# Kernel optimization log

Hardware: AMD Instinct MI355X
Metric: run time of the kernel (lower is better)

Reference implementation:

```python
import jax, jax.numpy as jnp
import numpy as np

B, N, D_PTS, D_MODEL, K = 2, 8192, 3, 128, 16


def _gather(points, idx):
    # points: (B, N, C), idx: (B, M, K) -> (B, M, K, C)
    return jax.vmap(lambda p, i: p[i])(points, idx)


def setup_inputs() -> dict:
    key = jax.random.key(0)
    ks = jax.random.split(key, 20)

    def w(k, shape, fan_in):
        bound = 1.0 / np.sqrt(fan_in)
        return jax.random.uniform(k, shape, jnp.float32, -bound, bound)

    return {
        "xyz": jax.random.normal(ks[0], (B, D_PTS, N), jnp.float32),
        "features": jax.random.normal(ks[1], (B, D_PTS, N), jnp.float32),
        "fc1_w": w(ks[2], (D_MODEL, D_PTS), D_PTS),
        "fc1_b": w(ks[3], (D_MODEL,), D_PTS),
        "fc2_w": w(ks[4], (D_PTS, D_MODEL), D_MODEL),
        "fc2_b": w(ks[5], (D_PTS,), D_MODEL),
        "d1_w": w(ks[6], (D_MODEL, 3), 3),
        "d1_b": w(ks[7], (D_MODEL,), 3),
        "d2_w": w(ks[8], (D_MODEL, D_MODEL), D_MODEL),
        "d2_b": w(ks[9], (D_MODEL,), D_MODEL),
        "g1_w": w(ks[10], (D_MODEL, D_MODEL), D_MODEL),
        "g1_b": w(ks[11], (D_MODEL,), D_MODEL),
        "g2_w": w(ks[12], (D_MODEL, D_MODEL), D_MODEL),
        "g2_b": w(ks[13], (D_MODEL,), D_MODEL),
        "wq_w": w(ks[14], (D_MODEL, D_MODEL), D_MODEL),
        "wk_w": w(ks[15], (D_MODEL, D_MODEL), D_MODEL),
        "wv_w": w(ks[16], (D_MODEL, D_MODEL), D_MODEL),
    }


def reference(xyz, features, fc1_w, fc1_b, fc2_w, fc2_b,
              d1_w, d1_b, d2_w, d2_b, g1_w, g1_b, g2_w, g2_b,
              wq_w, wk_w, wv_w):
    xyz_p = jnp.swapaxes(xyz, 1, 2)        # (B, N, 3)
    feat = jnp.swapaxes(features, 1, 2)    # (B, N, d_points)

    # square_distance(xyz, xyz): ||a||^2 + ||b||^2 - 2 a.b
    sq = jnp.sum(xyz_p * xyz_p, axis=-1)   # (B, N)
    dists = sq[:, :, None] + sq[:, None, :] - 2.0 * jnp.einsum('bnc,bmc->bnm', xyz_p, xyz_p)
    _, knn_idx = jax.lax.top_k(-dists, K)  # (B, N, K) indices of k smallest dists

    knn_xyz = _gather(xyz_p, knn_idx)      # (B, N, K, 3)
    pre = feat

    x = feat @ fc1_w.T + fc1_b             # (B, N, d_model)
    q = x @ wq_w.T                         # (B, N, d_model)
    kg = _gather(x @ wk_w.T, knn_idx)      # (B, N, K, d_model)
    vg = _gather(x @ wv_w.T, knn_idx)      # (B, N, K, d_model)

    rel = xyz_p[:, :, None] - knn_xyz      # (B, N, K, 3)
    pos = jax.nn.relu(rel @ d1_w.T + d1_b) @ d2_w.T + d2_b          # fc_delta

    h = q[:, :, None] - kg + pos
    attn = jax.nn.relu(h @ g1_w.T + g1_b) @ g2_w.T + g2_b           # fc_gamma
    attn = jax.nn.softmax(attn / np.sqrt(D_MODEL), axis=-2)         # softmax over K

    res = jnp.einsum('bmnf,bmnf->bmf', attn, vg + pos)              # (B, N, d_model)
    res = res @ fc2_w.T + fc2_b + pre                               # (B, N, d_points)
    return jnp.swapaxes(res, 1, 2)                                  # (B, d_points, N)
```

## Files before the change

kernel.cpp:

```cpp
#include <hip/hip_runtime.h>
#include <cfloat>

#define NPTS 8192

typedef __attribute__((ext_vector_type(8))) short short8;
typedef __attribute__((ext_vector_type(4))) short short4v;
typedef __attribute__((ext_vector_type(4))) float f32x4;

__device__ inline unsigned short f2bf(float f) {
    unsigned u = __builtin_bit_cast(unsigned, f);
    u += 0x7fffu + ((u >> 16) & 1u);
    return (unsigned short)(u >> 16);
}
__device__ inline float bf2f(unsigned short h) {
    unsigned u = ((unsigned)h) << 16;
    return __builtin_bit_cast(float, u);
}

__global__ void prep_kernel(const float* __restrict__ d2_w,
                            const float* __restrict__ g1_w,
                            const float* __restrict__ g2_w,
                            unsigned short* __restrict__ wd2,
                            unsigned short* __restrict__ wg1,
                            unsigned short* __restrict__ wg2,
                            const float* __restrict__ xyz,
                            float4* __restrict__ candp,
                            const float* __restrict__ wq_w,
                            const float* __restrict__ wk_w,
                            const float* __restrict__ wv_w,
                            float* __restrict__ wqT,
                            float* __restrict__ wkT,
                            float* __restrict__ wvT)
{
    int i = blockIdx.x * 256 + threadIdx.x;
    if (i < 49152) {
        int sel = i >> 14, off = i & 16383;
        const float* s = (sel == 0) ? d2_w : (sel == 1) ? g1_w : g2_w;
        unsigned short* d = (sel == 0) ? wd2 : (sel == 1) ? wg1 : wg2;
        d[off] = f2bf(s[off]);
    } else if (i < 65536) {
        int j = i - 49152;
        int b = j >> 13, n = j & 8191;
        const float* xg = xyz + (long)b * 3 * NPTS;
        float x = xg[n], y = xg[NPTS + n], z = xg[2*NPTS + n];
        float4 c; c.x = x; c.y = y; c.z = z;
        c.w = fmaf(x, x, fmaf(y, y, z * z));
        candp[j] = c;
    } else if (i < 114688) {
        int idx = i - 65536;
        int sel = idx >> 14, off = idx & 16383;
        int k = off >> 7, c = off & 127;
        const float* s = (sel == 0) ? wq_w : (sel == 1) ? wk_w : wv_w;
        float* d = (sel == 0) ? wqT : (sel == 1) ? wkT : wvT;
        d[off] = s[c * 128 + k];
    }
}

__global__ __launch_bounds__(128, 2)
void proj_kernel(const float* __restrict__ feat,
                 const float* __restrict__ fc1_w, const float* __restrict__ fc1_b,
                 const float* __restrict__ wqT, const float* __restrict__ wkT,
                 const float* __restrict__ wvT,
                 unsigned short* __restrict__ qb, unsigned short* __restrict__ kbuf,
                 unsigned short* __restrict__ vbuf)
{
    __shared__ float fl[8][3];
    __shared__ float xl[8][128];
    const int c = threadIdx.x;
    const long base = (long)blockIdx.x * 8;

    if (c < 24) {
        int p = c / 3, d = c % 3;
        long pt = base + p;
        int b = (int)(pt >> 13), n = (int)(pt & 8191);
        fl[p][d] = feat[((long)b * 3 + d) * NPTS + n];
    }
    __syncthreads();

    float w0 = fc1_w[c*3+0], w1 = fc1_w[c*3+1], w2 = fc1_w[c*3+2], b0 = fc1_b[c];
    #pragma unroll
    for (int p = 0; p < 8; ++p)
        xl[p][c] = fmaf(w0, fl[p][0], fmaf(w1, fl[p][1], fmaf(w2, fl[p][2], b0)));
    __syncthreads();

    float aq[8], ak[8], av[8];
    #pragma unroll
    for (int p = 0; p < 8; ++p) { aq[p] = 0.f; ak[p] = 0.f; av[p] = 0.f; }

    for (int i4 = 0; i4 < 32; ++i4) {
        const int k0 = i4 * 4;
        float qa = wqT[(k0+0)*128 + c], qbw = wqT[(k0+1)*128 + c];
        float qc2 = wqT[(k0+2)*128 + c], qd = wqT[(k0+3)*128 + c];
        float ka = wkT[(k0+0)*128 + c], kbw = wkT[(k0+1)*128 + c];
        float kc2 = wkT[(k0+2)*128 + c], kd = wkT[(k0+3)*128 + c];
        float va = wvT[(k0+0)*128 + c], vbw = wvT[(k0+1)*128 + c];
        float vc2 = wvT[(k0+2)*128 + c], vd = wvT[(k0+3)*128 + c];
        #pragma unroll
        for (int p = 0; p < 8; ++p) {
            float4 x = *(const float4*)&xl[p][k0];
            aq[p] = fmaf(qa,x.x, fmaf(qbw,x.y, fmaf(qc2,x.z, fmaf(qd,x.w, aq[p]))));
            ak[p] = fmaf(ka,x.x, fmaf(kbw,x.y, fmaf(kc2,x.z, fmaf(kd,x.w, ak[p]))));
            av[p] = fmaf(va,x.x, fmaf(vbw,x.y, fmaf(vc2,x.z, fmaf(vd,x.w, av[p]))));
        }
    }
    const int perm = (c & 15) * 8 + (c >> 4);
    #pragma unroll
    for (int p = 0; p < 8; ++p) {
        long pt = base + p;
        qb[pt*128 + perm]   = f2bf(aq[p]);
        kbuf[pt*128 + perm] = f2bf(ak[p]);
        vbuf[pt*128 + perm] = f2bf(av[p]);
    }
}

#define KNB 120
#define KBBASE 952
#define KCAP 64

__global__ __launch_bounds__(512, 6)
void knn_part_kernel(const float4* __restrict__ cand,
                     float* __restrict__ part_d, int* __restrict__ part_i)
{
    __shared__ unsigned hist[KNB * 64];
    __shared__ float2   surv[64 * 65];
    __shared__ unsigned scnt[64];
    __shared__ int      bthr[64];

    const int t  = threadIdx.x;
    const int ql = t & 63, wv = t >> 6;
    const int wv_u = __builtin_amdgcn_readfirstlane(wv);
    const int qsg = blockIdx.x >> 1;
    const int ck  = blockIdx.x & 1;
    const int b_u = qsg >> 7;
    const int q   = qsg * 64 + ql;
    const int n   = q & 8191;

    const float4* cp = cand + (b_u << 13) + ck * 4096 + wv_u * 512;
    const int ibase = ck * 4096 + wv_u * 512;
    float4 qc = cand[(b_u << 13) + n];
    const float qx2 = -2.f * qc.x, qy2 = -2.f * qc.y, qz2 = -2.f * qc.z;
    const float qw = qc.w;

    for (int i = t; i < KNB * 64; i += 512) hist[i] = 0u;
    if (t < 64) scnt[t] = 0u;
    __syncthreads();

    auto dtil = [&](float4 c) {
        return fmaf(qx2, c.x, fmaf(qy2, c.y, fmaf(qz2, c.z, c.w + qw)));
    };
    auto binOf = [&](float d) {
        float dc = fmaxf(d, 1e-30f);
        int b = (int)(__builtin_bit_cast(unsigned, dc) >> 20) - KBBASE;
        return b < 0 ? 0 : (b > (KNB - 1) ? (KNB - 1) : b);
    };

    {
        unsigned* hq = hist + ql;
        float4 A[8], Bv[8];
        #pragma unroll
        for (int u = 0; u < 8; ++u) A[u] = cp[u];
        for (int m = 0; m < 512; m += 16) {
            #pragma unroll
            for (int u = 0; u < 8; ++u) Bv[u] = cp[m + 8 + u];
            #pragma unroll
            for (int u = 0; u < 8; ++u) {
                int bb = binOf(dtil(A[u]));
                atomicAdd(hq + bb * 64, 1u);
            }
            if (m + 16 < 512) {
                #pragma unroll
                for (int u = 0; u < 8; ++u) A[u] = cp[m + 16 + u];
            }
            #pragma unroll
            for (int u = 0; u < 8; ++u) {
                int bb = binOf(dtil(Bv[u]));
                atomicAdd(hq + bb * 64, 1u);
            }
        }
    }
    __syncthreads();

    if (t < 64) {
        int cum = 0, bs = 0;
        #pragma unroll 8
        for (int b = 0; b < KNB; ++b) {
            cum += (int)hist[b * 64 + t];
            bs += (cum < 16) ? 1 : 0;
        }
        bthr[t] = (bs >= KNB - 1) ? 0x7FFFFFFF : ((bs + KBBASE + 1) << 20);
    }
    __syncthreads();

    {
        const int mythr = bthr[ql];
        float4 A[8], Bv[8];
        #pragma unroll
        for (int u = 0; u < 8; ++u) A[u] = cp[u];
        for (int m = 0; m < 512; m += 16) {
            #pragma unroll
            for (int u = 0; u < 8; ++u) Bv[u] = cp[m + 8 + u];
            #pragma unroll
            for (int u = 0; u < 8; ++u) {
                float d = dtil(A[u]);
                if (__builtin_bit_cast(int, d) < mythr) {
                    unsigned s = atomicAdd(&scnt[ql], 1u);
                    if (s < (unsigned)KCAP) {
                        float2 e; e.x = d;
                        e.y = __builtin_bit_cast(float, ibase + m + u);
                        surv[ql * 65 + s] = e;
                    }
                }
            }
            if (m + 16 < 512) {
                #pragma unroll
                for (int u = 0; u < 8; ++u) A[u] = cp[m + 16 + u];
            }
            #pragma unroll
            for (int u = 0; u < 8; ++u) {
                float d = dtil(Bv[u]);
                if (__builtin_bit_cast(int, d) < mythr) {
                    unsigned s = atomicAdd(&scnt[ql], 1u);
                    if (s < (unsigned)KCAP) {
                        float2 e; e.x = d;
                        e.y = __builtin_bit_cast(float, ibase + m + 8 + u);
                        surv[ql * 65 + s] = e;
                    }
                }
            }
        }
    }
    __syncthreads();

    {
        const int q2 = t >> 3;
        const int s0 = t & 7;
        const unsigned cnt = min(scnt[q2], (unsigned)KCAP);
        const float2* sp = surv + q2 * 65;
        const long pb = ((long)(qsg * 64 + q2)) * 32 + ck * 16;
        for (unsigned s = s0; s < cnt; s += 8) {
            float2 e = sp[s];
            float d = e.x;
            int idx = __builtin_bit_cast(int, e.y);
            int rank = 0;
            #pragma unroll 8
            for (unsigned j = 0; j < cnt; ++j) {
                float2 f = sp[j];
                float dj = f.x;
                int ij = __builtin_bit_cast(int, f.y);
                rank += ((dj < d) || (dj == d && ij < idx)) ? 1 : 0;
            }
            if (rank < 16) {
                part_d[pb + rank] = d;
                part_i[pb + rank] = idx;
            }
        }
    }
}

__global__ __launch_bounds__(256, 4)
void knn_merge_kernel(const float* __restrict__ part_d,
                      const int* __restrict__ part_i, int* __restrict__ knn)
{
    __shared__ float sd[8][33];
    __shared__ int   si[8][33];
    const int t = threadIdx.x;
    const int qq = t >> 5, e = t & 31;
    const long q = (long)blockIdx.x * 8 + qq;
    float d = part_d[q * 32 + e];
    int idx = part_i[q * 32 + e];
    sd[qq][e] = d; si[qq][e] = idx;
    __syncthreads();
    int rank = 0;
    #pragma unroll
    for (int j = 0; j < 32; ++j) {
        float dj = sd[qq][j];
        rank += ((dj < d) || (dj == d && si[qq][j] < idx)) ? 1 : 0;
    }
    if (rank < 16) knn[q * 16 + rank] = idx;
}

__device__ inline int hswz(int r, int c) {
    return r * 128 + (c ^ ((r & 7) << 4));
}

__global__ __launch_bounds__(64, 2)
void attn_kernel(const float* __restrict__ xyz, const float* __restrict__ feat,
                 const float* __restrict__ d1_w, const float* __restrict__ d1_b,
                 const float* __restrict__ d2_b, const float* __restrict__ g1_b,
                 const float* __restrict__ g2_b,
                 const float* __restrict__ fc2_w, const float* __restrict__ fc2_b,
                 const unsigned short* __restrict__ qb,
                 const unsigned short* __restrict__ kb,
                 const unsigned short* __restrict__ vb,
                 const unsigned short* __restrict__ wd2,
                 const unsigned short* __restrict__ wg1,
                 const unsigned short* __restrict__ wg2,
                 const int* __restrict__ knn, float* __restrict__ out)
{
    __shared__ unsigned short hbuf[32 * 128];

    const int lane = threadIdx.x;
    const int quad = lane >> 4, l15 = lane & 15;
    const long pbase = (long)blockIdx.x * 2;
    const int b = (int)(pbase >> 13);
    const long bofs = (long)b * NPTS;

    int m = 0; float rx = 0.f, ry = 0.f, rz = 0.f;
    if (lane < 32) {
        m = knn[(pbase + (lane >> 4)) * 16 + (lane & 15)];
        int nn = (int)((pbase + (lane >> 4)) & 8191);
        const float* xg = xyz + (long)b * 3 * NPTS;
        rx = xg[nn]        - xg[m];
        ry = xg[NPTS+nn]   - xg[NPTS+m];
        rz = xg[2*NPTS+nn] - xg[2*NPTS+m];
    }

    int koff[8];
    #pragma unroll
    for (int mt = 0; mt < 2; ++mt)
        #pragma unroll
        for (int r = 0; r < 4; ++r) {
            int idxm = __shfl(m, mt*16 + quad*4 + r);
            koff[mt*4 + r] = (int)(bofs + idxm) * 128 + l15*8;
        }

    short8 qvv[2], kgv[2][4], vgv[2][4];
    #pragma unroll
    for (int mt = 0; mt < 2; ++mt) {
        qvv[mt] = *(const short8*)(qb + (size_t)(pbase + mt) * 128 + l15*8);
        #pragma unroll
        for (int r = 0; r < 4; ++r)
            kgv[mt][r] = *(const short8*)(kb + koff[mt*4 + r]);
    }

    {
        float w0[8], w1[8], w2[8], bb[8];
        #pragma unroll
        for (int k = 0; k < 8; ++k) {
            int c = l15*8 + k;
            w0[k] = d1_w[c*3]; w1[k] = d1_w[c*3+1]; w2[k] = d1_w[c*3+2];
            bb[k] = d1_b[c];
        }
        #pragma unroll
        for (int i = 0; i < 8; ++i) {
            int row = quad + 4*i;
            float sx = __shfl(rx, row), sy = __shfl(ry, row), sz = __shfl(rz, row);
            short8 hv;
            #pragma unroll
            for (int k = 0; k < 8; ++k) {
                float v = fmaf(w0[k], sx, fmaf(w1[k], sy, fmaf(w2[k], sz, bb[k])));
                hv[k] = (short)f2bf(fmaxf(v, 0.f));
            }
            *(short8*)&hbuf[hswz(row, l15*8)] = hv;
        }
    }

    short8 A[2][4];
    f32x4 acc[2];

    auto loadA = [&]() {
        #pragma unroll
        for (int mt = 0; mt < 2; ++mt)
            #pragma unroll
            for (int kk = 0; kk < 4; ++kk)
                A[mt][kk] = *(const short8*)&hbuf[hswz(mt*16 + l15, kk*32 + quad*8)];
    };

    unsigned posp[2][8][2];

    loadA();
    #pragma unroll
    for (int n0 = 0; n0 < 8; ++n0) {
        const unsigned short* wp = wd2 + (n0*16 + l15) * 128 + quad*8;
        short8 B0 = *(const short8*)(wp);
        short8 B1 = *(const short8*)(wp + 32);
        short8 B2 = *(const short8*)(wp + 64);
        short8 B3 = *(const short8*)(wp + 96);
        acc[0] = (f32x4){0.f,0.f,0.f,0.f};
        acc[1] = (f32x4){0.f,0.f,0.f,0.f};
        __builtin_amdgcn_s_setprio(1);
        #pragma unroll
        for (int mt = 0; mt < 2; ++mt) {
            acc[mt] = __builtin_amdgcn_mfma_f32_16x16x32_bf16(A[mt][0], B0, acc[mt], 0, 0, 0);
            acc[mt] = __builtin_amdgcn_mfma_f32_16x16x32_bf16(A[mt][1], B1, acc[mt], 0, 0, 0);
            acc[mt] = __builtin_amdgcn_mfma_f32_16x16x32_bf16(A[mt][2], B2, acc[mt], 0, 0, 0);
            acc[mt] = __builtin_amdgcn_mfma_f32_16x16x32_bf16(A[mt][3], B3, acc[mt], 0, 0, 0);
        }
        __builtin_amdgcn_s_setprio(0);
        int c = n0*16 + l15;
        float bb = d2_b[c];
        #pragma unroll
        for (int mt = 0; mt < 2; ++mt) {
            float qv = bf2f((unsigned short)qvv[mt][n0]);
            float p0 = acc[mt][0] + bb, p1 = acc[mt][1] + bb;
            float p2 = acc[mt][2] + bb, p3 = acc[mt][3] + bb;
            posp[mt][n0][0] = (unsigned)f2bf(p0) | ((unsigned)f2bf(p1) << 16);
            posp[mt][n0][1] = (unsigned)f2bf(p2) | ((unsigned)f2bf(p3) << 16);
            int rb = mt*16 + quad*4;
            hbuf[hswz(rb+0, c)] = f2bf(qv - bf2f((unsigned short)kgv[mt][0][n0]) + p0);
            hbuf[hswz(rb+1, c)] = f2bf(qv - bf2f((unsigned short)kgv[mt][1][n0]) + p1);
            hbuf[hswz(rb+2, c)] = f2bf(qv - bf2f((unsigned short)kgv[mt][2][n0]) + p2);
            hbuf[hswz(rb+3, c)] = f2bf(qv - bf2f((unsigned short)kgv[mt][3][n0]) + p3);
        }
    }

    loadA();
    #pragma unroll
    for (int n0 = 0; n0 < 8; ++n0) {
        const unsigned short* wp = wg1 + (n0*16 + l15) * 128 + quad*8;
        short8 B0 = *(const short8*)(wp);
        short8 B1 = *(const short8*)(wp + 32);
        short8 B2 = *(const short8*)(wp + 64);
        short8 B3 = *(const short8*)(wp + 96);
        acc[0] = (f32x4){0.f,0.f,0.f,0.f};
        acc[1] = (f32x4){0.f,0.f,0.f,0.f};
        __builtin_amdgcn_s_setprio(1);
        #pragma unroll
        for (int mt = 0; mt < 2; ++mt) {
            acc[mt] = __builtin_amdgcn_mfma_f32_16x16x32_bf16(A[mt][0], B0, acc[mt], 0, 0, 0);
            acc[mt] = __builtin_amdgcn_mfma_f32_16x16x32_bf16(A[mt][1], B1, acc[mt], 0, 0, 0);
            acc[mt] = __builtin_amdgcn_mfma_f32_16x16x32_bf16(A[mt][2], B2, acc[mt], 0, 0, 0);
            acc[mt] = __builtin_amdgcn_mfma_f32_16x16x32_bf16(A[mt][3], B3, acc[mt], 0, 0, 0);
        }
        __builtin_amdgcn_s_setprio(0);
        int c = n0*16 + l15;
        float bb = g1_b[c];
        #pragma unroll
        for (int mt = 0; mt < 2; ++mt) {
            int rb = mt*16 + quad*4;
            #pragma unroll
            for (int r = 0; r < 4; ++r)
                hbuf[hswz(rb+r, c)] = f2bf(fmaxf(acc[mt][r] + bb, 0.f));
        }
    }

    #pragma unroll
    for (int mt = 0; mt < 2; ++mt)
        #pragma unroll
        for (int r = 0; r < 4; ++r)
            vgv[mt][r] = *(const short8*)(vb + koff[mt*4 + r]);

    loadA();
    const float sc = 0.08838834764831845f;
    float pr[2][3];
    #pragma unroll
    for (int mt = 0; mt < 2; ++mt) { pr[mt][0] = 0.f; pr[mt][1] = 0.f; pr[mt][2] = 0.f; }
    #pragma unroll
    for (int n0 = 0; n0 < 8; ++n0) {
        const unsigned short* wp = wg2 + (n0*16 + l15) * 128 + quad*8;
        short8 B0 = *(const short8*)(wp);
        short8 B1 = *(const short8*)(wp + 32);
        short8 B2 = *(const short8*)(wp + 64);
        short8 B3 = *(const short8*)(wp + 96);
        acc[0] = (f32x4){0.f,0.f,0.f,0.f};
        acc[1] = (f32x4){0.f,0.f,0.f,0.f};
        __builtin_amdgcn_s_setprio(1);
        #pragma unroll
        for (int mt = 0; mt < 2; ++mt) {
            acc[mt] = __builtin_amdgcn_mfma_f32_16x16x32_bf16(A[mt][0], B0, acc[mt], 0, 0, 0);
            acc[mt] = __builtin_amdgcn_mfma_f32_16x16x32_bf16(A[mt][1], B1, acc[mt], 0, 0, 0);
            acc[mt] = __builtin_amdgcn_mfma_f32_16x16x32_bf16(A[mt][2], B2, acc[mt], 0, 0, 0);
            acc[mt] = __builtin_amdgcn_mfma_f32_16x16x32_bf16(A[mt][3], B3, acc[mt], 0, 0, 0);
        }
        __builtin_amdgcn_s_setprio(0);
        int c = n0*16 + l15;
        float bb = g2_b[c];
        float f0 = fc2_w[c];
        float f1 = fc2_w[128 + c];
        float f2 = fc2_w[256 + c];
        #pragma unroll
        for (int mt = 0; mt < 2; ++mt) {
            float e0 = (acc[mt][0] + bb) * sc;
            float e1 = (acc[mt][1] + bb) * sc;
            float e2 = (acc[mt][2] + bb) * sc;
            float e3 = (acc[mt][3] + bb) * sc;
            float mx = fmaxf(fmaxf(e0, e1), fmaxf(e2, e3));
            mx = fmaxf(mx, __shfl_xor(mx, 16));
            mx = fmaxf(mx, __shfl_xor(mx, 32));
            e0 = __expf(e0 - mx); e1 = __expf(e1 - mx);
            e2 = __expf(e2 - mx); e3 = __expf(e3 - mx);
            float ssum = e0 + e1 + e2 + e3;
            ssum += __shfl_xor(ssum, 16);
            ssum += __shfl_xor(ssum, 32);
            float p0 = bf2f((unsigned short)(posp[mt][n0][0] & 0xffff));
            float p1 = bf2f((unsigned short)(posp[mt][n0][0] >> 16));
            float p2 = bf2f((unsigned short)(posp[mt][n0][1] & 0xffff));
            float p3 = bf2f((unsigned short)(posp[mt][n0][1] >> 16));
            float p = e0 * (bf2f((unsigned short)vgv[mt][0][n0]) + p0)
                    + e1 * (bf2f((unsigned short)vgv[mt][1][n0]) + p1)
                    + e2 * (bf2f((unsigned short)vgv[mt][2][n0]) + p2)
                    + e3 * (bf2f((unsigned short)vgv[mt][3][n0]) + p3);
            p += __shfl_xor(p, 16);
            p += __shfl_xor(p, 32);
            float rres = p / ssum;
            pr[mt][0] = fmaf(f0, rres, pr[mt][0]);
            pr[mt][1] = fmaf(f1, rres, pr[mt][1]);
            pr[mt][2] = fmaf(f2, rres, pr[mt][2]);
        }
    }

    #pragma unroll
    for (int mt = 0; mt < 2; ++mt) {
        float pr0 = pr[mt][0], pr1 = pr[mt][1], pr2 = pr[mt][2];
        #pragma unroll
        for (int s2 = 1; s2 <= 8; s2 <<= 1) {
            pr0 += __shfl_xor(pr0, s2);
            pr1 += __shfl_xor(pr1, s2);
            pr2 += __shfl_xor(pr2, s2);
        }
        int nn = (int)((pbase + mt) & 8191);
        if (lane < 3) {
            float pv = (lane == 0) ? pr0 : (lane == 1) ? pr1 : pr2;
            long o = ((long)b*3 + lane) * NPTS + nn;
            out[o] = pv + fc2_b[lane] + feat[o];
        }
    }
}

extern "C" void kernel_launch(void* const* d_in, const int* in_sizes, int n_in,
                              void* d_out, int out_size, void* d_ws, size_t ws_size,
                              hipStream_t stream)
{
    const float* xyz   = (const float*)d_in[0];
    const float* feat  = (const float*)d_in[1];
    const float* fc1_w = (const float*)d_in[2];
    const float* fc1_b = (const float*)d_in[3];
    const float* fc2_w = (const float*)d_in[4];
    const float* fc2_b = (const float*)d_in[5];
    const float* d1_w  = (const float*)d_in[6];
    const float* d1_b  = (const float*)d_in[7];
    const float* d2_w  = (const float*)d_in[8];
    const float* d2_b  = (const float*)d_in[9];
    const float* g1_w  = (const float*)d_in[10];
    const float* g1_b  = (const float*)d_in[11];
    const float* g2_w  = (const float*)d_in[12];
    const float* g2_b  = (const float*)d_in[13];
    const float* wq_w  = (const float*)d_in[14];
    const float* wk_w  = (const float*)d_in[15];
    const float* wv_w  = (const float*)d_in[16];
    float* out = (float*)d_out;

    unsigned short* qb  = (unsigned short*)d_ws;
    unsigned short* kb  = qb + (size_t)16384*128;
    unsigned short* vb  = kb + (size_t)16384*128;
    unsigned short* wd2 = vb + (size_t)16384*128;
    unsigned short* wg1 = wd2 + 16384;
    unsigned short* wg2 = wg1 + 16384;
    int*   knn_ws = (int*)(wg2 + 16384);
    float4* cand  = (float4*)(knn_ws + (size_t)16384*16);
    float* part_d = (float*)(cand + 16384);
    int*   part_i = (int*)(part_d + (size_t)16384*64);
    float* wqT    = part_d + (size_t)16384*32;
    float* wkT    = wqT + 16384;
    float* wvT    = wkT + 16384;

    hipLaunchKernelGGL(prep_kernel, dim3(448), dim3(256), 0, stream,
                       d2_w, g1_w, g2_w, wd2, wg1, wg2, xyz, cand,
                       wq_w, wk_w, wv_w, wqT, wkT, wvT);
    hipLaunchKernelGGL(knn_part_kernel, dim3(512), dim3(512), 0, stream,
                       cand, part_d, part_i);
    hipLaunchKernelGGL(knn_merge_kernel, dim3(2048), dim3(256), 0, stream,
                       part_d, part_i, knn_ws);
    hipLaunchKernelGGL(proj_kernel, dim3(2048), dim3(128), 0, stream,
                       feat, fc1_w, fc1_b, wqT, wkT, wvT, qb, kb, vb);
    hipLaunchKernelGGL(attn_kernel, dim3(8192), dim3(64), 0, stream,
                       xyz, feat, d1_w, d1_b, d2_b, g1_b, g2_b, fc2_w, fc2_b,
                       qb, kb, vb, wd2, wg1, wg2, knn_ws, out);
}
```

Measured before the change: 313.6 us.

## Merge kNN partial search and QKV projection into one heterogeneous launch

Fuses the kNN partial kernel and the QKV projection kernel into a single launch. The first 512 blocks do kNN and the remaining 512 blocks do the projection, with 4 groups of 8 points per block and shared memory unioned between the two roles. The aim is to run the independent projection work alongside kNN and drop one launch. In exchange, launch bounds drop from 6 to 2 blocks per CU for the kNN part, which may reduce its occupancy, and the projection blocks now carry the larger shared-memory footprint.

New measurement: 296.6 us. 5.4% less time.

```diff
diff --git a/kernel.cpp b/kernel.cpp
--- a/kernel.cpp
+++ b/kernel.cpp
@@ -56,203 +56,222 @@
     }
 }
 
-__global__ __launch_bounds__(128, 2)
-void proj_kernel(const float* __restrict__ feat,
-                 const float* __restrict__ fc1_w, const float* __restrict__ fc1_b,
-                 const float* __restrict__ wqT, const float* __restrict__ wkT,
-                 const float* __restrict__ wvT,
-                 unsigned short* __restrict__ qb, unsigned short* __restrict__ kbuf,
-                 unsigned short* __restrict__ vbuf)
-{
-    __shared__ float fl[8][3];
-    __shared__ float xl[8][128];
-    const int c = threadIdx.x;
-    const long base = (long)blockIdx.x * 8;
-
-    if (c < 24) {
-        int p = c / 3, d = c % 3;
-        long pt = base + p;
-        int b = (int)(pt >> 13), n = (int)(pt & 8191);
-        fl[p][d] = feat[((long)b * 3 + d) * NPTS + n];
-    }
-    __syncthreads();
-
-    float w0 = fc1_w[c*3+0], w1 = fc1_w[c*3+1], w2 = fc1_w[c*3+2], b0 = fc1_b[c];
-    #pragma unroll
-    for (int p = 0; p < 8; ++p)
-        xl[p][c] = fmaf(w0, fl[p][0], fmaf(w1, fl[p][1], fmaf(w2, fl[p][2], b0)));
-    __syncthreads();
-
-    float aq[8], ak[8], av[8];
-    #pragma unroll
-    for (int p = 0; p < 8; ++p) { aq[p] = 0.f; ak[p] = 0.f; av[p] = 0.f; }
-
-    for (int i4 = 0; i4 < 32; ++i4) {
-        const int k0 = i4 * 4;
-        float qa = wqT[(k0+0)*128 + c], qbw = wqT[(k0+1)*128 + c];
-        float qc2 = wqT[(k0+2)*128 + c], qd = wqT[(k0+3)*128 + c];
-        float ka = wkT[(k0+0)*128 + c], kbw = wkT[(k0+1)*128 + c];
-        float kc2 = wkT[(k0+2)*128 + c], kd = wkT[(k0+3)*128 + c];
-        float va = wvT[(k0+0)*128 + c], vbw = wvT[(k0+1)*128 + c];
-        float vc2 = wvT[(k0+2)*128 + c], vd = wvT[(k0+3)*128 + c];
-        #pragma unroll
-        for (int p = 0; p < 8; ++p) {
-            float4 x = *(const float4*)&xl[p][k0];
-            aq[p] = fmaf(qa,x.x, fmaf(qbw,x.y, fmaf(qc2,x.z, fmaf(qd,x.w, aq[p]))));
-            ak[p] = fmaf(ka,x.x, fmaf(kbw,x.y, fmaf(kc2,x.z, fmaf(kd,x.w, ak[p]))));
-            av[p] = fmaf(va,x.x, fmaf(vbw,x.y, fmaf(vc2,x.z, fmaf(vd,x.w, av[p]))));
-        }
-    }
-    const int perm = (c & 15) * 8 + (c >> 4);
-    #pragma unroll
-    for (int p = 0; p < 8; ++p) {
-        long pt = base + p;
-        qb[pt*128 + perm]   = f2bf(aq[p]);
-        kbuf[pt*128 + perm] = f2bf(ak[p]);
-        vbuf[pt*128 + perm] = f2bf(av[p]);
-    }
-}
-
 #define KNB 120
 #define KBBASE 952
 #define KCAP 64
 
-__global__ __launch_bounds__(512, 6)
-void knn_part_kernel(const float4* __restrict__ cand,
-                     float* __restrict__ part_d, int* __restrict__ part_i)
+__global__ __launch_bounds__(512, 2)
+void knn_proj_kernel(const float4* __restrict__ cand,
+                     float* __restrict__ part_d, int* __restrict__ part_i,
+                     const float* __restrict__ feat,
+                     const float* __restrict__ fc1_w, const float* __restrict__ fc1_b,
+                     const float* __restrict__ wqT, const float* __restrict__ wkT,
+                     const float* __restrict__ wvT,
+                     unsigned short* __restrict__ qb,
+                     unsigned short* __restrict__ kbuf,
+                     unsigned short* __restrict__ vbuf)
 {
-    __shared__ unsigned hist[KNB * 64];
-    __shared__ float2   surv[64 * 65];
-    __shared__ unsigned scnt[64];
-    __shared__ int      bthr[64];
-
-    const int t  = threadIdx.x;
-    const int ql = t & 63, wv = t >> 6;
-    const int wv_u = __builtin_amdgcn_readfirstlane(wv);
-    const int qsg = blockIdx.x >> 1;
-    const int ck  = blockIdx.x & 1;
-    const int b_u = qsg >> 7;
-    const int q   = qsg * 64 + ql;
-    const int n   = q & 8191;
-
-    const float4* cp = cand + (b_u << 13) + ck * 4096 + wv_u * 512;
-    const int ibase = ck * 4096 + wv_u * 512;
-    float4 qc = cand[(b_u << 13) + n];
-    const float qx2 = -2.f * qc.x, qy2 = -2.f * qc.y, qz2 = -2.f * qc.z;
-    const float qw = qc.w;
-
-    for (int i = t; i < KNB * 64; i += 512) hist[i] = 0u;
-    if (t < 64) scnt[t] = 0u;
-    __syncthreads();
-
-    auto dtil = [&](float4 c) {
-        return fmaf(qx2, c.x, fmaf(qy2, c.y, fmaf(qz2, c.z, c.w + qw)));
-    };
-    auto binOf = [&](float d) {
-        float dc = fmaxf(d, 1e-30f);
-        int b = (int)(__builtin_bit_cast(unsigned, dc) >> 20) - KBBASE;
-        return b < 0 ? 0 : (b > (KNB - 1) ? (KNB - 1) : b);
-    };
-
-    {
-        unsigned* hq = hist + ql;
-        float4 A[8], Bv[8];
-        #pragma unroll
-        for (int u = 0; u < 8; ++u) A[u] = cp[u];
-        for (int m = 0; m < 512; m += 16) {
+    __shared__ union {
+        struct {
+            unsigned hist[KNB * 64];
+            float2   surv[64 * 65];
+            unsigned scnt[64];
+            int      bthr[64];
+        } k;
+        struct {
+            float fl[32][3];
+            float xl[32][128];
+        } p;
+    } sm;
+
+    const int t = threadIdx.x;
+
+    if (blockIdx.x < 512) {
+        unsigned* hist = sm.k.hist;
+        float2*   surv = sm.k.surv;
+        unsigned* scnt = sm.k.scnt;
+        int*      bthr = sm.k.bthr;
+
+        const int ql = t & 63, wv = t >> 6;
+        const int wv_u = __builtin_amdgcn_readfirstlane(wv);
+        const int qsg = blockIdx.x >> 1;
+        const int ck  = blockIdx.x & 1;
+        const int b_u = qsg >> 7;
+        const int q   = qsg * 64 + ql;
+        const int n   = q & 8191;
+
+        const float4* cp = cand + (b_u << 13) + ck * 4096 + wv_u * 512;
+        const int ibase = ck * 4096 + wv_u * 512;
+        float4 qc = cand[(b_u << 13) + n];
+        const float qx2 = -2.f * qc.x, qy2 = -2.f * qc.y, qz2 = -2.f * qc.z;
+        const float qw = qc.w;
+
+        for (int i = t; i < KNB * 64; i += 512) hist[i] = 0u;
+        if (t < 64) scnt[t] = 0u;
+        __syncthreads();
+
+        auto dtil = [&](float4 c) {
+            return fmaf(qx2, c.x, fmaf(qy2, c.y, fmaf(qz2, c.z, c.w + qw)));
+        };
+        auto binOf = [&](float d) {
+            float dc = fmaxf(d, 1e-30f);
+            int b = (int)(__builtin_bit_cast(unsigned, dc) >> 20) - KBBASE;
+            return b < 0 ? 0 : (b > (KNB - 1) ? (KNB - 1) : b);
+        };
+
+        {
+            unsigned* hq = hist + ql;
+            float4 A[8], Bv[8];
             #pragma unroll
-            for (int u = 0; u < 8; ++u) Bv[u] = cp[m + 8 + u];
+            for (int u = 0; u < 8; ++u) A[u] = cp[u];
+            for (int m = 0; m < 512; m += 16) {
+                #pragma unroll
+                for (int u = 0; u < 8; ++u) Bv[u] = cp[m + 8 + u];
+                #pragma unroll
+                for (int u = 0; u < 8; ++u) {
+                    int bb = binOf(dtil(A[u]));
+                    atomicAdd(hq + bb * 64, 1u);
+                }
+                if (m + 16 < 512) {
+                    #pragma unroll
+                    for (int u = 0; u < 8; ++u) A[u] = cp[m + 16 + u];
+                }
+                #pragma unroll
+                for (int u = 0; u < 8; ++u) {
+                    int bb = binOf(dtil(Bv[u]));
+                    atomicAdd(hq + bb * 64, 1u);
+                }
+            }
+        }
+        __syncthreads();
+
+        if (t < 64) {
+            int cum = 0, bs = 0;
+            #pragma unroll 8
+            for (int b = 0; b < KNB; ++b) {
+                cum += (int)hist[b * 64 + t];
+                bs += (cum < 16) ? 1 : 0;
+            }
+            bthr[t] = (bs >= KNB - 1) ? 0x7FFFFFFF : ((bs + KBBASE + 1) << 20);
+        }
+        __syncthreads();
+
+        {
+            const int mythr = bthr[ql];
+            float4 A[8], Bv[8];
             #pragma unroll
-            for (int u = 0; u < 8; ++u) {
-                int bb = binOf(dtil(A[u]));
-                atomicAdd(hq + bb * 64, 1u);
+            for (int u = 0; u < 8; ++u) A[u] = cp[u];
+            for (int m = 0; m < 512; m += 16) {
+                #pragma unroll
+                for (int u = 0; u < 8; ++u) Bv[u] = cp[m + 8 + u];
+                #pragma unroll
+                for (int u = 0; u < 8; ++u) {
+                    float d = dtil(A[u]);
+                    if (__builtin_bit_cast(int, d) < mythr) {
+                        unsigned s = atomicAdd(&scnt[ql], 1u);
+                        if (s < (unsigned)KCAP) {
+                            float2 e; e.x = d;
+                            e.y = __builtin_bit_cast(float, ibase + m + u);
+                            surv[ql * 65 + s] = e;
+                        }
+                    }
+                }
+                if (m + 16 < 512) {
+                    #pragma unroll
+                    for (int u = 0; u < 8; ++u) A[u] = cp[m + 16 + u];
+                }
+                #pragma unroll
+                for (int u = 0; u < 8; ++u) {
+                    float d = dtil(Bv[u]);
+                    if (__builtin_bit_cast(int, d) < mythr) {
+                        unsigned s = atomicAdd(&scnt[ql], 1u);
+                        if (s < (unsigned)KCAP) {
+                            float2 e; e.x = d;
+                            e.y = __builtin_bit_cast(float, ibase + m + 8 + u);
+                            surv[ql * 65 + s] = e;
+                        }
+                    }
+                }
             }
-            if (m + 16 < 512) {
-                #pragma unroll
-                for (int u = 0; u < 8; ++u) A[u] = cp[m + 16 + u];
+        }
+        __syncthreads();
+
+        {
+            const int q2 = t >> 3;
+            const int s0 = t & 7;
+            const unsigned cnt = min(scnt[q2], (unsigned)KCAP);
+            const float2* sp = surv + q2 * 65;
+            const long pb = ((long)(qsg * 64 + q2)) * 32 + ck * 16;
+            for (unsigned s = s0; s < cnt; s += 8) {
+                float2 e = sp[s];
+                float d = e.x;
+                int idx = __builtin_bit_cast(int, e.y);
+                int rank = 0;
+                #pragma unroll 8
+                for (unsigned j = 0; j < cnt; ++j) {
+                    float2 f = sp[j];
+                    float dj = f.x;
+                    int ij = __builtin_bit_cast(int, f.y);
+                    rank += ((dj < d) || (dj == d && ij < idx)) ? 1 : 0;
+                }
+                if (rank < 16) {
+                    part_d[pb + rank] = d;
+                    part_i[pb + rank] = idx;
+                }
             }
+        }
+    } else {
+        float (*fl)[3]   = sm.p.fl;
+        float (*xl)[128] = sm.p.xl;
+
+        const int tc = t & 127;
+        const int pg = t >> 7;
+        const long base = (long)(blockIdx.x - 512) * 32 + pg * 8;
+
+        if (tc < 24) {
+            int p = tc / 3, d = tc % 3;
+            long pt = base + p;
+            int b = (int)(pt >> 13), n = (int)(pt & 8191);
+            fl[pg*8 + p][d] = feat[((long)b * 3 + d) * NPTS + n];
+        }
+        __syncthreads();
+
+        float w0 = fc1_w[tc*3+0], w1 = fc1_w[tc*3+1], w2 = fc1_w[tc*3+2];
+        float b0 = fc1_b[tc];
+        #pragma unroll
+        for (int p = 0; p < 8; ++p)
+            xl[pg*8 + p][tc] = fmaf(w0, fl[pg*8+p][0],
+                               fmaf(w1, fl[pg*8+p][1],
+                               fmaf(w2, fl[pg*8+p][2], b0)));
+        __syncthreads();
+
+        float aq[8], ak[8], av[8];
+        #pragma unroll
+        for (int p = 0; p < 8; ++p) { aq[p] = 0.f; ak[p] = 0.f; av[p] = 0.f; }
+
+        for (int i4 = 0; i4 < 32; ++i4) {
+            const int k0 = i4 * 4;
+            float qa = wqT[(k0+0)*128 + tc], qbw = wqT[(k0+1)*128 + tc];
+            float qc2 = wqT[(k0+2)*128 + tc], qd = wqT[(k0+3)*128 + tc];
+            float ka = wkT[(k0+0)*128 + tc], kbw = wkT[(k0+1)*128 + tc];
+            float kc2 = wkT[(k0+2)*128 + tc], kd = wkT[(k0+3)*128 + tc];
+            float va = wvT[(k0+0)*128 + tc], vbw = wvT[(k0+1)*128 + tc];
+            float vc2 = wvT[(k0+2)*128 + tc], vd = wvT[(k0+3)*128 + tc];
             #pragma unroll
-            for (int u = 0; u < 8; ++u) {
-                int bb = binOf(dtil(Bv[u]));
-                atomicAdd(hq + bb * 64, 1u);
+            for (int p = 0; p < 8; ++p) {
+                float4 x = *(const float4*)&xl[pg*8 + p][k0];
+                aq[p] = fmaf(qa,x.x, fmaf(qbw,x.y, fmaf(qc2,x.z, fmaf(qd,x.w, aq[p]))));
+                ak[p] = fmaf(ka,x.x, fmaf(kbw,x.y, fmaf(kc2,x.z, fmaf(kd,x.w, ak[p]))));
+                av[p] = fmaf(va,x.x, fmaf(vbw,x.y, fmaf(vc2,x.z, fmaf(vd,x.w, av[p]))));
             }
         }
-    }
-    __syncthreads();
-
-    if (t < 64) {
-        int cum = 0, bs = 0;
-        #pragma unroll 8
-        for (int b = 0; b < KNB; ++b) {
-            cum += (int)hist[b * 64 + t];
-            bs += (cum < 16) ? 1 : 0;
-        }
-        bthr[t] = (bs >= KNB - 1) ? 0x7FFFFFFF : ((bs + KBBASE + 1) << 20);
-    }
-    __syncthreads();
-
-    {
-        const int mythr = bthr[ql];
-        float4 A[8], Bv[8];
-        #pragma unroll
-        for (int u = 0; u < 8; ++u) A[u] = cp[u];
-        for (int m = 0; m < 512; m += 16) {
-            #pragma unroll
-            for (int u = 0; u < 8; ++u) Bv[u] = cp[m + 8 + u];
-            #pragma unroll
-            for (int u = 0; u < 8; ++u) {
-                float d = dtil(A[u]);
-                if (__builtin_bit_cast(int, d) < mythr) {
-                    unsigned s = atomicAdd(&scnt[ql], 1u);
-                    if (s < (unsigned)KCAP) {
-                        float2 e; e.x = d;
-                        e.y = __builtin_bit_cast(float, ibase + m + u);
-                        surv[ql * 65 + s] = e;
-                    }
-                }
-            }
-            if (m + 16 < 512) {
-                #pragma unroll
-                for (int u = 0; u < 8; ++u) A[u] = cp[m + 16 + u];
-            }
-            #pragma unroll
-            for (int u = 0; u < 8; ++u) {
-                float d = dtil(Bv[u]);
-                if (__builtin_bit_cast(int, d) < mythr) {
-                    unsigned s = atomicAdd(&scnt[ql], 1u);
-                    if (s < (unsigned)KCAP) {
-                        float2 e; e.x = d;
-                        e.y = __builtin_bit_cast(float, ibase + m + 8 + u);
-                        surv[ql * 65 + s] = e;
-                    }
-                }
-            }
-        }
-    }
-    __syncthreads();
-
-    {
-        const int q2 = t >> 3;
-        const int s0 = t & 7;
-        const unsigned cnt = min(scnt[q2], (unsigned)KCAP);
-        const float2* sp = surv + q2 * 65;
-        const long pb = ((long)(qsg * 64 + q2)) * 32 + ck * 16;
-        for (unsigned s = s0; s < cnt; s += 8) {
-            float2 e = sp[s];
-            float d = e.x;
-            int idx = __builtin_bit_cast(int, e.y);
-            int rank = 0;
-            #pragma unroll 8
-            for (unsigned j = 0; j < cnt; ++j) {
-                float2 f = sp[j];
-                float dj = f.x;
-                int ij = __builtin_bit_cast(int, f.y);
-                rank += ((dj < d) || (dj == d && ij < idx)) ? 1 : 0;
-            }
-            if (rank < 16) {
-                part_d[pb + rank] = d;
-                part_i[pb + rank] = idx;
-            }
+        const int perm = (tc & 15) * 8 + (tc >> 4);
+        #pragma unroll
+        for (int p = 0; p < 8; ++p) {
+            long pt = base + p;
+            qb[pt*128 + perm]   = f2bf(aq[p]);
+            kbuf[pt*128 + perm] = f2bf(ak[p]);
+            vbuf[pt*128 + perm] = f2bf(av[p]);
         }
     }
 }
@@ -557,12 +576,11 @@
     hipLaunchKernelGGL(prep_kernel, dim3(448), dim3(256), 0, stream,
                        d2_w, g1_w, g2_w, wd2, wg1, wg2, xyz, cand,
                        wq_w, wk_w, wv_w, wqT, wkT, wvT);
-    hipLaunchKernelGGL(knn_part_kernel, dim3(512), dim3(512), 0, stream,
-                       cand, part_d, part_i);
+    hipLaunchKernelGGL(knn_proj_kernel, dim3(1024), dim3(512), 0, stream,
+                       cand, part_d, part_i,
+                       feat, fc1_w, fc1_b, wqT, wkT, wvT, qb, kb, vb);
     hipLaunchKernelGGL(knn_merge_kernel, dim3(2048), dim3(256), 0, stream,
                        part_d, part_i, knn_ws);
-    hipLaunchKernelGGL(proj_kernel, dim3(2048), dim3(128), 0, stream,
-                       feat, fc1_w, fc1_b, wqT, wkT, wvT, qb, kb, vb);
     hipLaunchKernelGGL(attn_kernel, dim3(8192), dim3(64), 0, stream,
                        xyz, feat, d1_w, d1_b, d2_b, g1_b, g2_b, fc2_w, fc2_b,
                        qb, kb, vb, wd2, wg1, wg2, knn_ws, out);
```
